# Performance work log

Hardware: AMD Instinct MI355X
Metric: run time of the kernel (lower is better)

Reference implementation:

```python
import jax, jax.numpy as jnp
import numpy as np

H = 48  # hidden_size


def _lstm_cell(inp, h, c, Wih, Whh, bih, bhh):
    # PyTorch LSTMCell: gates ordered (i, f, g, o)
    gates = inp @ Wih.T + h @ Whh.T + bih + bhh
    i, f, g, o = jnp.split(gates, 4, axis=-1)
    i = jax.nn.sigmoid(i)
    f = jax.nn.sigmoid(f)
    g = jnp.tanh(g)
    o = jax.nn.sigmoid(o)
    c_new = f * c + i * g
    h_new = o * jnp.tanh(c_new)
    return h_new, c_new


def setup_inputs() -> dict:
    key = jax.random.key(0)
    ks = jax.random.split(key, 8)
    B, T = 4096, 512
    s = 0.1
    return {
        "x": jax.random.normal(ks[0], (B, T), dtype=jnp.float32),
        "W_ih0": jax.random.normal(ks[1], (4 * H, 1), dtype=jnp.float32) * s,
        "W_hh0": jax.random.normal(ks[2], (4 * H, H), dtype=jnp.float32) * s,
        "b_ih0": jnp.full((4 * H,), 0.01, dtype=jnp.float32),
        "b_hh0": jnp.full((4 * H,), 0.01, dtype=jnp.float32),
        "W_ih1": jax.random.normal(ks[3], (4 * H, H), dtype=jnp.float32) * s,
        "W_hh1": jax.random.normal(ks[4], (4 * H, H), dtype=jnp.float32) * s,
        "b_ih1": jnp.full((4 * H,), 0.01, dtype=jnp.float32),
        "b_hh1": jnp.full((4 * H,), 0.01, dtype=jnp.float32),
        "W_lin": jax.random.normal(ks[5], (1, H), dtype=jnp.float32) * s,
        "b_lin": jnp.full((1,), 0.01, dtype=jnp.float32),
        "future_pred": 64,
    }


def reference(x, W_ih0, W_hh0, b_ih0, b_hh0, W_ih1, W_hh1, b_ih1, b_hh1,
              W_lin, b_lin, future_pred):
    B = x.shape[0]
    h0 = jnp.zeros((B, H), dtype=jnp.float32)
    c0 = jnp.zeros((B, H), dtype=jnp.float32)
    h1 = jnp.zeros((B, H), dtype=jnp.float32)
    c1 = jnp.zeros((B, H), dtype=jnp.float32)

    def tick(h0, c0, h1, c1, inp):  # inp: [B,1]
        h0, c0 = _lstm_cell(inp, h0, c0, W_ih0, W_hh0, b_ih0, b_hh0)
        h1, c1 = _lstm_cell(h0, h1, c1, W_ih1, W_hh1, b_ih1, b_hh1)
        out = h1 @ W_lin.T + b_lin  # [B,1]
        return h0, c0, h1, c1, out

    # teacher-forced pass over observed sequence
    def step_obs(carry, xt):
        h0, c0, h1, c1 = carry
        h0, c0, h1, c1, out = tick(h0, c0, h1, c1, xt)
        return (h0, c0, h1, c1), out

    xs = jnp.swapaxes(x, 0, 1)[:, :, None]  # [T, B, 1]
    (h0, c0, h1, c1), outs_obs = jax.lax.scan(step_obs, (h0, c0, h1, c1), xs)
    last_out = outs_obs[-1]

    def step_fut(carry, _):
        h0, c0, h1, c1, out = carry
        h0, c0, h1, c1, out = tick(h0, c0, h1, c1, out)
        return (h0, c0, h1, c1, out), out

    _, outs_fut = jax.lax.scan(step_fut, (h0, c0, h1, c1, last_out), None,
                               length=future_pred)

    outs = jnp.concatenate([outs_obs, outs_fut], axis=0)  # [T+F, B, 1]
    return jnp.swapaxes(outs[:, :, 0], 0, 1)  # [B, T+F]
```

## Files before the change

kernel.cpp:

```cpp
#include <hip/hip_runtime.h>

#define T_OBS 512
#define NTILE 2
#define NWAVE 12
#define RSTRH 200
#define PSTR  28
#define L2E   1.44269504089f

typedef float    f32x4 __attribute__((ext_vector_type(4)));
typedef _Float16 f16x8 __attribute__((ext_vector_type(8)));

#define MF(A,B,C) __builtin_amdgcn_mfma_f32_16x16x32_f16(A, B, C, 0, 0, 0)

__device__ __forceinline__ float lstm_act(const f32x4 a, float& c) {
    const float Ei = __builtin_amdgcn_exp2f(a[0]);
    const float Ef = __builtin_amdgcn_exp2f(a[1]);
    const float Eg = __builtin_amdgcn_exp2f(a[2]);
    const float Eo = __builtin_amdgcn_exp2f(a[3]);
    const float ui = 1.f + Ei, uf = 1.f + Ef, ug = 1.f + Eg, uo = 1.f + Eo;
    const float r1 = __builtin_amdgcn_rcpf(ui * uf);
    const float ig = r1 * uf;
    const float fg = r1 * ui;
    const float r2 = __builtin_amdgcn_rcpf(ug * uo);
    const float og = r2 * ug;
    const float gg = fmaf(r2 * uo, -2.f, 1.f);
    c = fg * c + ig * gg;
    const float Ec = __builtin_amdgcn_exp2f(2.f * L2E * c);
    const float th = fmaf(__builtin_amdgcn_rcpf(1.f + Ec), -2.f, 1.f);
    return og * th;
}

__global__ __launch_bounds__(768, 1) void lstm2_v6(
    const float* __restrict__ x,
    const float* __restrict__ Wih0, const float* __restrict__ Whh0,
    const float* __restrict__ bih0, const float* __restrict__ bhh0,
    const float* __restrict__ Wih1, const float* __restrict__ Whh1,
    const float* __restrict__ bih1, const float* __restrict__ bhh1,
    const float* __restrict__ Wlin, const float* __restrict__ blin,
    const int* __restrict__ fut,
    float* __restrict__ out)
{
    __shared__ __attribute__((aligned(16))) _Float16 s_h[16 * RSTRH];
    __shared__ __attribute__((aligned(16))) float s_pr[2][16 * PSTR];

    const int tid  = threadIdx.x;
    const int wave = tid >> 6;
    const int lane = tid & 63;
    const int n    = lane & 15;
    const int rg   = lane >> 4;
    const bool isL1 = (wave >= 6);
    const int  w    = isL1 ? (wave - 6) : wave;

    for (int i = tid; i < 16 * RSTRH; i += 768) s_h[i] = (_Float16)0.f;

    const float sgl = ((n & 3) == 2) ? 2.f * L2E : -L2E;

    f16x8 ah[NTILE][3], al[NTILE][3];
    #pragma unroll
    for (int i = 0; i < NTILE; ++i) {
        const int m  = NTILE * w + i;
        const int rp = 16 * m + n;
        const int r0 = (rp & 3) * 48 + (rp >> 2);
        #pragma unroll
        for (int s = 0; s < 3; ++s)
            #pragma unroll
            for (int j = 0; j < 8; ++j) {
                const int k = 32 * s + 8 * rg + j;
                float v;
                if (isL1) v = ((k < 48) ? Wih1[r0 * 48 + k] : Whh1[r0 * 48 + (k - 48)]) * sgl;
                else      v = (s < 2 && k < 48) ? Whh0[r0 * 48 + k] * sgl : 0.f;
                const _Float16 hi = (_Float16)v;
                ah[i][s][j] = hi;
                al[i][s][j] = (_Float16)(v - (float)hi);
            }
    }

    const float sg4[4] = { -L2E, -L2E, 2.f * L2E, -L2E };
    f32x4 bv[NTILE], wi0v[NTILE];
    float wlq[NTILE];
    int   hu[NTILE];
    #pragma unroll
    for (int i = 0; i < NTILE; ++i) {
        const int u = 4 * (NTILE * w + i) + rg;
        hu[i]  = u;
        wlq[i] = Wlin[u];
        #pragma unroll
        for (int g = 0; g < 4; ++g) {
            bv[i][g]   = (isL1 ? (bih1[g * 48 + u] + bhh1[g * 48 + u])
                               : (bih0[g * 48 + u] + bhh0[g * 48 + u])) * sg4[g];
            wi0v[i][g] = Wih0[g * 48 + u] * sg4[g];
        }
    }

    int koff[3];
    #pragma unroll
    for (int s = 0; s < 3; ++s) {
        const int k0 = 32 * s + 8 * rg;
        koff[s] = (k0 < 48) ? k0 : k0 + 48;
    }

    const int F    = fut[0];
    const int TT   = T_OBS + F;
    const int bb0  = blockIdx.x * 16;
    const float bl = blin[0];
    const int xrow = (bb0 + n) * T_OBS;
    const int nb   = n * RSTRH;
    const int prh  = n * PSTR + w * 4 + rg;

    float cc[NTILE];
    #pragma unroll
    for (int i = 0; i < NTILE; ++i) cc[i] = 0.f;

    const f32x4 z4 = { 0.f, 0.f, 0.f, 0.f };

    __syncthreads();

    if (!isL1) {
        const float x0 = x[xrow];
        #pragma unroll
        for (int i = 0; i < NTILE; ++i) {
            const f32x4 a = bv[i] + wi0v[i] * x0;
            s_h[nb + hu[i]] = (_Float16)lstm_act(a, cc[i]);
        }
    }
    __syncthreads();

    float xcur = 0.f;
    if (!isL1) xcur = x[xrow + 1];

#define STEADY(TAU_, CB_, PB_) do {                                              \
    if (!isL1) {                                                                 \
        const float xnxt = x[xrow + (((TAU_) + 1 < T_OBS) ? (TAU_) + 1 : T_OBS - 1)]; \
        if ((TAU_) >= 2 && tid < 16) {                                           \
            const float* pr = &s_pr[((TAU_) - 1) & 1][tid * PSTR];               \
            const f32x4 sv = *(const f32x4*)(pr)      + *(const f32x4*)(pr + 4)  \
                           + *(const f32x4*)(pr + 8)  + *(const f32x4*)(pr + 12) \
                           + *(const f32x4*)(pr + 16) + *(const f32x4*)(pr + 20);\
            out[(bb0 + tid) * TT + ((TAU_) - 2)] = sv[0]+sv[1]+sv[2]+sv[3]+bl;   \
        }                                                                        \
        const f16x8 bh0 = *(const f16x8*)(s_h + nb + (PB_) + koff[0]);           \
        const f16x8 bh1 = *(const f16x8*)(s_h + nb + (PB_) + koff[1]);           \
        f32x4 Aq[NTILE], Bq[NTILE];                                              \
        _Pragma("unroll")                                                        \
        for (int i = 0; i < NTILE; ++i) {                                        \
            Aq[i] = MF(ah[i][0], bh0, bv[i]);                                    \
            Aq[i] = MF(al[i][0], bh0, Aq[i]);                                    \
            Bq[i] = MF(ah[i][1], bh1, z4);                                       \
            Bq[i] = MF(al[i][1], bh1, Bq[i]);                                    \
        }                                                                        \
        _Pragma("unroll")                                                        \
        for (int i = 0; i < NTILE; ++i) {                                        \
            const f32x4 a = Aq[i] + Bq[i] + wi0v[i] * xcur;                      \
            s_h[nb + (CB_) + hu[i]] = (_Float16)lstm_act(a, cc[i]);              \
        }                                                                        \
        xcur = xnxt;                                                             \
    } else {                                                                     \
        const f16x8 bh0 = *(const f16x8*)(s_h + nb + (PB_) + koff[0]);           \
        const f16x8 bh1 = *(const f16x8*)(s_h + nb + (PB_) + koff[1]);           \
        const f16x8 bh2 = *(const f16x8*)(s_h + nb + (PB_) + koff[2]);           \
        f32x4 Aq[NTILE], Bq[NTILE];                                              \
        _Pragma("unroll")                                                        \
        for (int i = 0; i < NTILE; ++i) {                                        \
            Aq[i] = MF(ah[i][0], bh0, bv[i]);                                    \
            Aq[i] = MF(al[i][0], bh0, Aq[i]);                                    \
            Aq[i] = MF(ah[i][1], bh1, Aq[i]);                                    \
            Bq[i] = MF(al[i][1], bh1, z4);                                       \
            Bq[i] = MF(ah[i][2], bh2, Bq[i]);                                    \
            Bq[i] = MF(al[i][2], bh2, Bq[i]);                                    \
        }                                                                        \
        float part = 0.f;                                                        \
        _Pragma("unroll")                                                        \
        for (int i = 0; i < NTILE; ++i) {                                        \
            const f32x4 a = Aq[i] + Bq[i];                                       \
            const float h = lstm_act(a, cc[i]);                                  \
            s_h[nb + 96 + (CB_) + hu[i]] = (_Float16)h;                          \
            part = fmaf(h, wlq[i], part);                                        \
        }                                                                        \
        s_pr[(TAU_) & 1][prh] = part;                                            \
    }                                                                            \
    __syncthreads();                                                             \
} while (0)

    for (int tau = 1; tau < T_OBS - 1; tau += 2) {
        STEADY(tau,     48, 0);
        STEADY(tau + 1,  0, 48);
    }
    STEADY(T_OBS - 1, 48, 0);

    if (tid < 16) {
        const float* pr = &s_pr[1][tid * PSTR];
        const f32x4 sv = *(const f32x4*)(pr)      + *(const f32x4*)(pr + 4)
                       + *(const f32x4*)(pr + 8)  + *(const f32x4*)(pr + 12)
                       + *(const f32x4*)(pr + 16) + *(const f32x4*)(pr + 20);
        out[(bb0 + tid) * TT + (T_OBS - 2)] = sv[0] + sv[1] + sv[2] + sv[3] + bl;
    }

    for (int tau = T_OBS; tau <= TT; ++tau) {
        const int cb = (tau & 1) * 48;
        const int pb = 48 - cb;
        const int rb = nb + pb;

        f32x4 Aq[NTILE], Bq[NTILE];
        if (isL1) {
            f16x8 bh[3];
            #pragma unroll
            for (int s = 0; s < 3; ++s) bh[s] = *(const f16x8*)(s_h + rb + koff[s]);
            #pragma unroll
            for (int i = 0; i < NTILE; ++i) {
                Aq[i] = MF(ah[i][0], bh[0], bv[i]);
                Aq[i] = MF(al[i][0], bh[0], Aq[i]);
                Aq[i] = MF(ah[i][1], bh[1], Aq[i]);
                Bq[i] = MF(al[i][1], bh[1], z4);
                Bq[i] = MF(ah[i][2], bh[2], Bq[i]);
                Bq[i] = MF(al[i][2], bh[2], Bq[i]);
            }
            float part = 0.f;
            #pragma unroll
            for (int i = 0; i < NTILE; ++i) {
                const f32x4 a = Aq[i] + Bq[i];
                const float h = lstm_act(a, cc[i]);
                s_h[nb + 96 + cb + hu[i]] = (_Float16)h;
                part = fmaf(h, wlq[i], part);
            }
            s_pr[tau & 1][prh] = part;
        } else {
            const f16x8 bh0 = *(const f16x8*)(s_h + rb + koff[0]);
            const f16x8 bh1 = *(const f16x8*)(s_h + rb + koff[1]);
            #pragma unroll
            for (int i = 0; i < NTILE; ++i) {
                Aq[i] = MF(ah[i][0], bh0, bv[i]);
                Aq[i] = MF(al[i][0], bh0, Aq[i]);
                Bq[i] = MF(ah[i][1], bh1, z4);
                Bq[i] = MF(al[i][1], bh1, Bq[i]);
            }
        }
        __syncthreads();

        if (!isL1) {
            const float* pr = &s_pr[tau & 1][n * PSTR];
            const f32x4 sv = *(const f32x4*)(pr)      + *(const f32x4*)(pr + 4)
                           + *(const f32x4*)(pr + 8)  + *(const f32x4*)(pr + 12)
                           + *(const f32x4*)(pr + 16) + *(const f32x4*)(pr + 20);
            const float o = sv[0] + sv[1] + sv[2] + sv[3] + bl;
            if (tid < 16) out[(bb0 + n) * TT + (tau - 1)] = o;
            if (tau < TT) {
                #pragma unroll
                for (int i = 0; i < NTILE; ++i) {
                    const f32x4 a = Aq[i] + Bq[i] + wi0v[i] * o;
                    s_h[nb + cb + hu[i]] = (_Float16)lstm_act(a, cc[i]);
                }
            }
        }
        __syncthreads();
    }
}

extern "C" void kernel_launch(void* const* d_in, const int* in_sizes, int n_in,
                              void* d_out, int out_size, void* d_ws, size_t ws_size,
                              hipStream_t stream) {
    const float* x    = (const float*)d_in[0];
    const float* Wih0 = (const float*)d_in[1];
    const float* Whh0 = (const float*)d_in[2];
    const float* bih0 = (const float*)d_in[3];
    const float* bhh0 = (const float*)d_in[4];
    const float* Wih1 = (const float*)d_in[5];
    const float* Whh1 = (const float*)d_in[6];
    const float* bih1 = (const float*)d_in[7];
    const float* bhh1 = (const float*)d_in[8];
    const float* Wlin = (const float*)d_in[9];
    const float* blin = (const float*)d_in[10];
    const int*   fut  = (const int*)d_in[11];
    float* out = (float*)d_out;

    const int B    = in_sizes[0] / T_OBS;
    const int grid = B / 16;
    lstm2_v6<<<grid, 768, 0, stream>>>(
        x, Wih0, Whh0, bih0, bhh0, Wih1, Whh1, bih1, bhh1, Wlin, blin, fut, out);
}
```

Baseline: 544.3 us.

## Permute hidden layout to pack paired fp16 writes and merge activation reciprocals

Permutes the K ordering of the weight fragments so each lane's two hidden units sit next to each other in LDS. Each lane then stores both as one packed 32-bit write instead of two 16-bit writes, and the row stride is padded to 264 with the layer-1 region at offset 128. The activation function now uses one reciprocal for all four gates instead of two. The observed-phase output reduction is spread across a full wave using shuffles instead of 16 threads doing vector sums. These changes aim to shorten the serial per-step critical path, at the cost of a single reciprocal over a larger product, which risks overflow when gate inputs are large.

```diff
diff --git a/kernel.cpp b/kernel.cpp
--- a/kernel.cpp
+++ b/kernel.cpp
@@ -1,36 +1,39 @@
 #include <hip/hip_runtime.h>
 
 #define T_OBS 512
-#define NTILE 2
-#define NWAVE 12
-#define RSTRH 200
+#define RSTRH 264
 #define PSTR  28
 #define L2E   1.44269504089f
 
 typedef float    f32x4 __attribute__((ext_vector_type(4)));
 typedef _Float16 f16x8 __attribute__((ext_vector_type(8)));
 
-#define MF(A,B,C) __builtin_amdgcn_mfma_f32_16x16x32_f16(A, B, C, 0, 0, 0)
-
-__device__ __forceinline__ float lstm_act(const f32x4 a, float& c) {
-    const float Ei = __builtin_amdgcn_exp2f(a[0]);
-    const float Ef = __builtin_amdgcn_exp2f(a[1]);
-    const float Eg = __builtin_amdgcn_exp2f(a[2]);
-    const float Eo = __builtin_amdgcn_exp2f(a[3]);
-    const float ui = 1.f + Ei, uf = 1.f + Ef, ug = 1.f + Eg, uo = 1.f + Eo;
-    const float r1 = __builtin_amdgcn_rcpf(ui * uf);
-    const float ig = r1 * uf;
-    const float fg = r1 * ui;
-    const float r2 = __builtin_amdgcn_rcpf(ug * uo);
-    const float og = r2 * ug;
-    const float gg = fmaf(r2 * uo, -2.f, 1.f);
-    c = fg * c + ig * gg;
-    const float Ec = __builtin_amdgcn_exp2f(2.f * L2E * c);
-    const float th = fmaf(__builtin_amdgcn_rcpf(1.f + Ec), -2.f, 1.f);
-    return og * th;
-}
-
-__global__ __launch_bounds__(768, 1) void lstm2_v6(
+#define MF(A,B,C) __builtin_amdgcn_mfma_f32_16x16x32_f16(A,B,C,0,0,0)
+
+__device__ __forceinline__ unsigned f2h(float f){
+    union { _Float16 h; unsigned short u; } v; v.h=(_Float16)f; return (unsigned)v.u;
+}
+
+__device__ __forceinline__ float act1(const f32x4 a, float& c){
+    const float Ei=__builtin_amdgcn_exp2f(a[0]), Ef=__builtin_amdgcn_exp2f(a[1]);
+    const float Eg=__builtin_amdgcn_exp2f(a[2]), Eo=__builtin_amdgcn_exp2f(a[3]);
+    const float ui=1.f+Ei, uf=1.f+Ef, ug=1.f+Eg, uo=1.f+Eo;
+    const float P=ui*uf, Q=ug*uo;
+    const float R=__builtin_amdgcn_rcpf(P*Q);
+    const float aP=R*Q, aQ=R*P;
+    const float ig=aP*uf, fg=aP*ui;
+    const float og=aQ*ug;
+    const float gg=fmaf(aQ*uo,-2.f,1.f);
+    c = fg*c + ig*gg;
+    const float Ec=__builtin_amdgcn_exp2f(2.f*L2E*c);
+    return og*fmaf(__builtin_amdgcn_rcpf(1.f+Ec),-2.f,1.f);
+}
+
+__device__ __forceinline__ int u_of_pos(const int p){
+    return 8*(p>>3) + 4*(p&1) + ((p&7)>>1);
+}
+
+__global__ __launch_bounds__(768, 1) void lstm2_v8(
     const float* __restrict__ x,
     const float* __restrict__ Wih0, const float* __restrict__ Whh0,
     const float* __restrict__ bih0, const float* __restrict__ bhh0,
@@ -42,33 +45,33 @@
 {
     __shared__ __attribute__((aligned(16))) _Float16 s_h[16 * RSTRH];
     __shared__ __attribute__((aligned(16))) float s_pr[2][16 * PSTR];
+    unsigned* const s32 = (unsigned*)s_h;
 
     const int tid  = threadIdx.x;
-    const int wave = tid >> 6;
-    const int lane = tid & 63;
-    const int n    = lane & 15;
-    const int rg   = lane >> 4;
+    const int wave = tid >> 6, lane = tid & 63;
+    const int q    = lane & 15, rg = lane >> 4;
     const bool isL1 = (wave >= 6);
-    const int  w    = isL1 ? (wave - 6) : wave;
+    const int  w    = isL1 ? wave - 6 : wave;
 
     for (int i = tid; i < 16 * RSTRH; i += 768) s_h[i] = (_Float16)0.f;
 
-    const float sgl = ((n & 3) == 2) ? 2.f * L2E : -L2E;
-
-    f16x8 ah[NTILE][3], al[NTILE][3];
+    const float sgl = ((q & 3) == 2) ? 2.f * L2E : -L2E;
+
+    f16x8 ah[2][3], al[2][3];
     #pragma unroll
-    for (int i = 0; i < NTILE; ++i) {
-        const int m  = NTILE * w + i;
-        const int rp = 16 * m + n;
+    for (int i = 0; i < 2; ++i) {
+        const int t  = 2 * w + i;
+        const int rp = 16 * t + q;
         const int r0 = (rp & 3) * 48 + (rp >> 2);
         #pragma unroll
         for (int s = 0; s < 3; ++s)
             #pragma unroll
             for (int j = 0; j < 8; ++j) {
-                const int k = 32 * s + 8 * rg + j;
-                float v;
-                if (isL1) v = ((k < 48) ? Wih1[r0 * 48 + k] : Whh1[r0 * 48 + (k - 48)]) * sgl;
-                else      v = (s < 2 && k < 48) ? Whh0[r0 * 48 + k] * sgl : 0.f;
+                const int p = 32 * s + 8 * rg + j;
+                float v = 0.f;
+                if (isL1) v = ((p < 48) ? Wih1[r0 * 48 + u_of_pos(p)]
+                                        : Whh1[r0 * 48 + u_of_pos(p - 48)]) * sgl;
+                else if (p < 48) v = Whh0[r0 * 48 + u_of_pos(p)] * sgl;
                 const _Float16 hi = (_Float16)v;
                 ah[i][s][j] = hi;
                 al[i][s][j] = (_Float16)(v - (float)hi);
@@ -76,18 +79,16 @@
     }
 
     const float sg4[4] = { -L2E, -L2E, 2.f * L2E, -L2E };
-    f32x4 bv[NTILE], wi0v[NTILE];
-    float wlq[NTILE];
-    int   hu[NTILE];
+    f32x4 bvt[2], wi0v[2];
+    float wlq[2];
     #pragma unroll
-    for (int i = 0; i < NTILE; ++i) {
-        const int u = 4 * (NTILE * w + i) + rg;
-        hu[i]  = u;
+    for (int i = 0; i < 2; ++i) {
+        const int u = 8 * w + 4 * i + rg;
         wlq[i] = Wlin[u];
         #pragma unroll
         for (int g = 0; g < 4; ++g) {
-            bv[i][g]   = (isL1 ? (bih1[g * 48 + u] + bhh1[g * 48 + u])
-                               : (bih0[g * 48 + u] + bhh0[g * 48 + u])) * sg4[g];
+            bvt[i][g]  = (isL1 ? (bih1[g*48+u] + bhh1[g*48+u])
+                               : (bih0[g*48+u] + bhh0[g*48+u])) * sg4[g];
             wi0v[i][g] = Wih0[g * 48 + u] * sg4[g];
         }
     }
@@ -95,97 +96,91 @@
     int koff[3];
     #pragma unroll
     for (int s = 0; s < 3; ++s) {
-        const int k0 = 32 * s + 8 * rg;
-        koff[s] = (k0 < 48) ? k0 : k0 + 48;
+        const int p0 = 32 * s + 8 * rg;
+        koff[s] = p0 + ((p0 >= 48) ? 80 : 0);
     }
 
     const int F    = fut[0];
     const int TT   = T_OBS + F;
     const int bb0  = blockIdx.x * 16;
     const float bl = blin[0];
-    const int xrow = (bb0 + n) * T_OBS;
-    const int nb   = n * RSTRH;
-    const int prh  = n * PSTR + w * 4 + rg;
-
-    float cc[NTILE];
-    #pragma unroll
-    for (int i = 0; i < NTILE; ++i) cc[i] = 0.f;
-
+    const int xrow = (bb0 + q) * T_OBS;
+    const int nbh  = q * RSTRH;
+    const int hwp  = nbh + (isL1 ? 128 : 0) + 8 * w + 2 * rg;
+    const int prw  = q * PSTR + 4 * w + rg;
+
+    float cc0 = 0.f, cc1 = 0.f;
     const f32x4 z4 = { 0.f, 0.f, 0.f, 0.f };
 
     __syncthreads();
 
     if (!isL1) {
         const float x0 = x[xrow];
-        #pragma unroll
-        for (int i = 0; i < NTILE; ++i) {
-            const f32x4 a = bv[i] + wi0v[i] * x0;
-            s_h[nb + hu[i]] = (_Float16)lstm_act(a, cc[i]);
-        }
+        const f32x4 a0 = bvt[0] + wi0v[0] * x0;
+        const f32x4 a1 = bvt[1] + wi0v[1] * x0;
+        const unsigned h0 = f2h(act1(a0, cc0));
+        const unsigned h1 = f2h(act1(a1, cc1));
+        s32[hwp >> 1] = h0 | (h1 << 16);
     }
     __syncthreads();
-
-    float xcur = 0.f;
-    if (!isL1) xcur = x[xrow + 1];
+    float xcur = isL1 ? 0.f : x[xrow + 1];
 
 #define STEADY(TAU_, CB_, PB_) do {                                              \
     if (!isL1) {                                                                 \
         const float xnxt = x[xrow + (((TAU_) + 1 < T_OBS) ? (TAU_) + 1 : T_OBS - 1)]; \
-        if ((TAU_) >= 2 && tid < 16) {                                           \
-            const float* pr = &s_pr[((TAU_) - 1) & 1][tid * PSTR];               \
-            const f32x4 sv = *(const f32x4*)(pr)      + *(const f32x4*)(pr + 4)  \
-                           + *(const f32x4*)(pr + 8)  + *(const f32x4*)(pr + 12) \
-                           + *(const f32x4*)(pr + 16) + *(const f32x4*)(pr + 20);\
-            out[(bb0 + tid) * TT + ((TAU_) - 2)] = sv[0]+sv[1]+sv[2]+sv[3]+bl;   \
+        if ((TAU_) >= 2 && wave == 0) {           \
+            const int nn = lane >> 2, j0 = lane & 3;                             \
+            const float* pr = &s_pr[((TAU_) - 1) & 1][nn * PSTR];                \
+            float sg = pr[j0] + pr[j0+4] + pr[j0+8] + pr[j0+12]                  \
+                     + pr[j0+16] + pr[j0+20];                                    \
+            sg += __shfl_xor(sg, 1); sg += __shfl_xor(sg, 2);                    \
+            if (j0 == 0) out[(bb0 + nn) * TT + ((TAU_) - 2)] = sg + bl;          \
         }                                                                        \
-        const f16x8 bh0 = *(const f16x8*)(s_h + nb + (PB_) + koff[0]);           \
-        const f16x8 bh1 = *(const f16x8*)(s_h + nb + (PB_) + koff[1]);           \
-        f32x4 Aq[NTILE], Bq[NTILE];                                              \
+        const f16x8 B0 = *(const f16x8*)(s_h + nbh + (PB_) + koff[0]);           \
+        const f16x8 B1 = *(const f16x8*)(s_h + nbh + (PB_) + koff[1]);           \
+        f32x4 Aq[2], Bq[2];                                                      \
         _Pragma("unroll")                                                        \
-        for (int i = 0; i < NTILE; ++i) {                                        \
-            Aq[i] = MF(ah[i][0], bh0, bv[i]);                                    \
-            Aq[i] = MF(al[i][0], bh0, Aq[i]);                                    \
-            Bq[i] = MF(ah[i][1], bh1, z4);                                       \
-            Bq[i] = MF(al[i][1], bh1, Bq[i]);                                    \
+        for (int i = 0; i < 2; ++i) {                                            \
+            Aq[i] = MF(ah[i][0], B0, bvt[i]);                                    \
+            Aq[i] = MF(al[i][0], B0, Aq[i]);                                     \
+            Bq[i] = MF(ah[i][1], B1, z4);                                        \
+            Bq[i] = MF(al[i][1], B1, Bq[i]);                                     \
         }                                                                        \
-        _Pragma("unroll")                                                        \
-        for (int i = 0; i < NTILE; ++i) {                                        \
-            const f32x4 a = Aq[i] + Bq[i] + wi0v[i] * xcur;                      \
-            s_h[nb + (CB_) + hu[i]] = (_Float16)lstm_act(a, cc[i]);              \
-        }                                                                        \
+        const f32x4 a0 = Aq[0] + Bq[0] + wi0v[0] * xcur;                         \
+        const f32x4 a1 = Aq[1] + Bq[1] + wi0v[1] * xcur;                         \
+        const unsigned h0 = f2h(act1(a0, cc0));                                  \
+        const unsigned h1 = f2h(act1(a1, cc1));                                  \
+        s32[(hwp + (CB_)) >> 1] = h0 | (h1 << 16);                               \
         xcur = xnxt;                                                             \
     } else {                                                                     \
-        const f16x8 bh0 = *(const f16x8*)(s_h + nb + (PB_) + koff[0]);           \
-        const f16x8 bh1 = *(const f16x8*)(s_h + nb + (PB_) + koff[1]);           \
-        const f16x8 bh2 = *(const f16x8*)(s_h + nb + (PB_) + koff[2]);           \
-        f32x4 Aq[NTILE], Bq[NTILE];                                              \
+        const f16x8 B0 = *(const f16x8*)(s_h + nbh + (PB_) + koff[0]);           \
+        const f16x8 B1 = *(const f16x8*)(s_h + nbh + (PB_) + koff[1]);           \
+        const f16x8 B2 = *(const f16x8*)(s_h + nbh + (PB_) + koff[2]);           \
+        f32x4 Aq[2], Bq[2];                                                      \
         _Pragma("unroll")                                                        \
-        for (int i = 0; i < NTILE; ++i) {                                        \
-            Aq[i] = MF(ah[i][0], bh0, bv[i]);                                    \
-            Aq[i] = MF(al[i][0], bh0, Aq[i]);                                    \
-            Aq[i] = MF(ah[i][1], bh1, Aq[i]);                                    \
-            Bq[i] = MF(al[i][1], bh1, z4);                                       \
-            Bq[i] = MF(ah[i][2], bh2, Bq[i]);                                    \
-            Bq[i] = MF(al[i][2], bh2, Bq[i]);                                    \
+        for (int i = 0; i < 2; ++i) {                                            \
+            Aq[i] = MF(ah[i][0], B0, bvt[i]);                                    \
+            Aq[i] = MF(al[i][0], B0, Aq[i]);                                     \
+            Aq[i] = MF(ah[i][1], B1, Aq[i]);                                     \
+            Bq[i] = MF(al[i][1], B1, z4);                                        \
+            Bq[i] = MF(ah[i][2], B2, Bq[i]);                                     \
+            Bq[i] = MF(al[i][2], B2, Bq[i]);                                     \
         }                                                                        \
-        float part = 0.f;                                                        \
-        _Pragma("unroll")                                                        \
-        for (int i = 0; i < NTILE; ++i) {                                        \
-            const f32x4 a = Aq[i] + Bq[i];                                       \
-            const float h = lstm_act(a, cc[i]);                                  \
-            s_h[nb + 96 + (CB_) + hu[i]] = (_Float16)h;                          \
-            part = fmaf(h, wlq[i], part);                                        \
-        }                                                                        \
-        s_pr[(TAU_) & 1][prh] = part;                                            \
+        const f32x4 a0 = Aq[0] + Bq[0];                                          \
+        const f32x4 a1 = Aq[1] + Bq[1];                                          \
+        const float h0 = act1(a0, cc0);                                          \
+        const float h1 = act1(a1, cc1);                                          \
+        s32[(hwp + (CB_)) >> 1] = f2h(h0) | (f2h(h1) << 16);                     \
+        s_pr[(TAU_) & 1][prw] = fmaf(h1, wlq[1], h0 * wlq[0]);                   \
     }                                                                            \
     __syncthreads();                                                             \
 } while (0)
 
     for (int tau = 1; tau < T_OBS - 1; tau += 2) {
-        STEADY(tau,     48, 0);
-        STEADY(tau + 1,  0, 48);
-    }
-    STEADY(T_OBS - 1, 48, 0);
+        STEADY(tau,     64, 0);
+        STEADY(tau + 1,  0, 64);
+    }
+    STEADY(T_OBS - 1, 64, 0);
 
     if (tid < 16) {
         const float* pr = &s_pr[1][tid * PSTR];
@@ -196,59 +191,55 @@
     }
 
     for (int tau = T_OBS; tau <= TT; ++tau) {
-        const int cb = (tau & 1) * 48;
-        const int pb = 48 - cb;
-        const int rb = nb + pb;
-
-        f32x4 Aq[NTILE], Bq[NTILE];
+        const int cb = (tau & 1) * 64;
+        const int pb = cb ^ 64;
+
+        f32x4 Aq[2], Bq[2];
         if (isL1) {
-            f16x8 bh[3];
+            const f16x8 B0 = *(const f16x8*)(s_h + nbh + pb + koff[0]);
+            const f16x8 B1 = *(const f16x8*)(s_h + nbh + pb + koff[1]);
+            const f16x8 B2 = *(const f16x8*)(s_h + nbh + pb + koff[2]);
             #pragma unroll
-            for (int s = 0; s < 3; ++s) bh[s] = *(const f16x8*)(s_h + rb + koff[s]);
+            for (int i = 0; i < 2; ++i) {
+                Aq[i] = MF(ah[i][0], B0, bvt[i]);
+                Aq[i] = MF(al[i][0], B0, Aq[i]);
+                Aq[i] = MF(ah[i][1], B1, Aq[i]);
+                Bq[i] = MF(al[i][1], B1, z4);
+                Bq[i] = MF(ah[i][2], B2, Bq[i]);
+                Bq[i] = MF(al[i][2], B2, Bq[i]);
+            }
+            const f32x4 a0 = Aq[0] + Bq[0];
+            const f32x4 a1 = Aq[1] + Bq[1];
+            const float h0 = act1(a0, cc0);
+            const float h1 = act1(a1, cc1);
+            s32[(hwp + cb) >> 1] = f2h(h0) | (f2h(h1) << 16);
+            s_pr[tau & 1][prw] = fmaf(h1, wlq[1], h0 * wlq[0]);
+        } else {
+            const f16x8 B0 = *(const f16x8*)(s_h + nbh + pb + koff[0]);
+            const f16x8 B1 = *(const f16x8*)(s_h + nbh + pb + koff[1]);
             #pragma unroll
-            for (int i = 0; i < NTILE; ++i) {
-                Aq[i] = MF(ah[i][0], bh[0], bv[i]);
-                Aq[i] = MF(al[i][0], bh[0], Aq[i]);
-                Aq[i] = MF(ah[i][1], bh[1], Aq[i]);
-                Bq[i] = MF(al[i][1], bh[1], z4);
-                Bq[i] = MF(ah[i][2], bh[2], Bq[i]);
-                Bq[i] = MF(al[i][2], bh[2], Bq[i]);
-            }
-            float part = 0.f;
-            #pragma unroll
-            for (int i = 0; i < NTILE; ++i) {
-                const f32x4 a = Aq[i] + Bq[i];
-                const float h = lstm_act(a, cc[i]);
-                s_h[nb + 96 + cb + hu[i]] = (_Float16)h;
-                part = fmaf(h, wlq[i], part);
-            }
-            s_pr[tau & 1][prh] = part;
-        } else {
-            const f16x8 bh0 = *(const f16x8*)(s_h + rb + koff[0]);
-            const f16x8 bh1 = *(const f16x8*)(s_h + rb + koff[1]);
-            #pragma unroll
-            for (int i = 0; i < NTILE; ++i) {
-                Aq[i] = MF(ah[i][0], bh0, bv[i]);
-                Aq[i] = MF(al[i][0], bh0, Aq[i]);
-                Bq[i] = MF(ah[i][1], bh1, z4);
-                Bq[i] = MF(al[i][1], bh1, Bq[i]);
+            for (int i = 0; i < 2; ++i) {
+                Aq[i] = MF(ah[i][0], B0, bvt[i]);
+                Aq[i] = MF(al[i][0], B0, Aq[i]);
+                Bq[i] = MF(ah[i][1], B1, z4);
+                Bq[i] = MF(al[i][1], B1, Bq[i]);
             }
         }
         __syncthreads();
 
         if (!isL1) {
-            const float* pr = &s_pr[tau & 1][n * PSTR];
+            const float* pr = &s_pr[tau & 1][q * PSTR];
             const f32x4 sv = *(const f32x4*)(pr)      + *(const f32x4*)(pr + 4)
                            + *(const f32x4*)(pr + 8)  + *(const f32x4*)(pr + 12)
                            + *(const f32x4*)(pr + 16) + *(const f32x4*)(pr + 20);
             const float o = sv[0] + sv[1] + sv[2] + sv[3] + bl;
-            if (tid < 16) out[(bb0 + n) * TT + (tau - 1)] = o;
+            if (tid < 16) out[(bb0 + q) * TT + (tau - 1)] = o;
             if (tau < TT) {
-                #pragma unroll
-                for (int i = 0; i < NTILE; ++i) {
-                    const f32x4 a = Aq[i] + Bq[i] + wi0v[i] * o;
-                    s_h[nb + cb + hu[i]] = (_Float16)lstm_act(a, cc[i]);
-                }
+                const f32x4 a0 = Aq[0] + Bq[0] + wi0v[0] * o;
+                const f32x4 a1 = Aq[1] + Bq[1] + wi0v[1] * o;
+                const unsigned h0 = f2h(act1(a0, cc0));
+                const unsigned h1 = f2h(act1(a1, cc1));
+                s32[(hwp + cb) >> 1] = h0 | (h1 << 16);
             }
         }
         __syncthreads();
@@ -274,6 +265,6 @@
 
     const int B    = in_sizes[0] / T_OBS;
     const int grid = B / 16;
-    lstm2_v6<<<grid, 768, 0, stream>>>(
+    lstm2_v8<<<grid, 768, 0, stream>>>(
         x, Wih0, Whh0, bih0, bhh0, Wih1, Whh1, bih1, bhh1, Wlin, blin, fut, out);
 }
```

New measurement: 512.9 us. 1.06x faster.
